# Kernel optimization log

Measured on AMD Instinct MI355X. Metric: run time of the kernel, lower is better.

## Reference

```python
import jax, jax.numpy as jnp
import numpy as np

EMB, HEADS, DEPTH, SEQ, BATCH = 256, 8, 4, 8192, 4
DH = EMB // HEADS  # 32
FF = 4 * EMB
EPS = 1e-5


def setup_inputs() -> dict:
    key = jax.random.key(0)
    ks = jax.random.split(key, 8)
    w = lambda k, shape: jax.random.normal(k, shape, dtype=jnp.float32) * 0.02
    D = DEPTH
    return {
        "x": jax.random.normal(ks[0], (BATCH, SEQ, EMB), dtype=jnp.float32),
        "Wq": w(ks[1], (D, EMB, EMB)),
        "Wk": w(ks[2], (D, EMB, EMB)),
        "Wv": w(ks[3], (D, EMB, EMB)),
        "Wo": w(ks[4], (D, EMB, EMB)),
        "bo": jnp.zeros((D, EMB), jnp.float32),
        "ln1_g": jnp.ones((D, EMB), jnp.float32),
        "ln1_b": jnp.zeros((D, EMB), jnp.float32),
        "W1": w(ks[5], (D, EMB, FF)),
        "b1": jnp.zeros((D, FF), jnp.float32),
        "W2": w(ks[6], (D, FF, EMB)),
        "b2": jnp.zeros((D, EMB), jnp.float32),
        "ln2_g": jnp.ones((D, EMB), jnp.float32),
        "ln2_b": jnp.zeros((D, EMB), jnp.float32),
    }


def _layernorm(x, g, b):
    mu = x.mean(-1, keepdims=True)
    var = ((x - mu) ** 2).mean(-1, keepdims=True)
    return (x - mu) * jax.lax.rsqrt(var + EPS) * g + b


def _linear_attn(x, Wq, Wk, Wv, Wo, bo):
    # lucidrains linear_attn: q,k scaled by d**-0.25; softmax q over feature dim,
    # k over sequence dim; context = k^T v (per head), out = q @ context.
    b, n, dm = x.shape
    split = lambda t: t.reshape(b, n, HEADS, DH).transpose(0, 2, 1, 3)  # -> bhnd
    scale = DH ** -0.25
    q = jax.nn.softmax(split(x @ Wq) * scale, axis=-1)   # over d
    k = jax.nn.softmax(split(x @ Wk) * scale, axis=-2)   # over n
    v = split(x @ Wv)
    context = jnp.einsum('bhnd,bhne->bhde', k, v)        # [b,h,d,d]
    out = jnp.einsum('bhnd,bhde->bhne', q, context)      # [b,h,n,d]
    out = out.transpose(0, 2, 1, 3).reshape(b, n, dm)
    return out @ Wo + bo


def _forward(x, Wq, Wk, Wv, Wo, bo, ln1_g, ln1_b, W1, b1, W2, b2, ln2_g, ln2_b):
    for i in range(DEPTH):
        h = _layernorm(x, ln1_g[i], ln1_b[i])
        x = x + _linear_attn(h, Wq[i], Wk[i], Wv[i], Wo[i], bo[i])
        h = _layernorm(x, ln2_g[i], ln2_b[i])
        x = x + (jax.nn.gelu(h @ W1[i] + b1[i], approximate=False) @ W2[i] + b2[i])
    return x


def reference(x, Wq, Wk, Wv, Wo, bo, ln1_g, ln1_b, W1, b1, W2, b2, ln2_g, ln2_b):
    return _forward(x, Wq, Wk, Wv, Wo, bo, ln1_g, ln1_b, W1, b1, W2, b2, ln2_g, ln2_b)
```

## Files before the change

kernel.cpp:

```cpp
#include <hip/hip_runtime.h>
#include <hip/hip_bf16.h>

typedef __attribute__((ext_vector_type(8))) short bf16x8;
typedef __attribute__((ext_vector_type(4))) float f32x4;

#define EMB 256
#define HEADS 8
#define DH 32
#define SEQ 8192
#define BATCH 4
#define NROWS (SEQ*BATCH)
#define FFD 1024
#define DEPTH 4
#define QKVN 768
#define SCALE 0.42044820762685725f
#define NCHUNK 128
#define ROWS_PER_CHUNK (SEQ/NCHUNK)

static __device__ __forceinline__ float bf2f(ushort u){
  union { unsigned int i; float f; } x; x.i = ((unsigned int)u) << 16; return x.f;
}
static __device__ __forceinline__ ushort f2bf(float f){
  union { __hip_bfloat16 h; ushort u; } cv;
  cv.h = __float2bfloat16(f);
  return cv.u;
}
static __device__ __forceinline__ float gelu_f(float v){
  float y = 0.7978845608028654f * (v + 0.044715f*v*v*v);
  float e = __expf(2.0f*y);
  return 0.5f*v*(1.0f + (1.0f - 2.0f/(e + 1.0f)));
}

static __device__ __forceinline__ void gload_lds16(const ushort* g, ushort* l){
  __builtin_amdgcn_global_load_lds(
      (const __attribute__((address_space(1))) unsigned int*)(uintptr_t)g,
      (__attribute__((address_space(3))) unsigned int*)(uintptr_t)l,
      16, 0, 0);
}

__global__ __launch_bounds__(256) void prep_weights(
    const float* __restrict__ Wq, const float* __restrict__ Wk,
    const float* __restrict__ Wv, const float* __restrict__ Wo,
    const float* __restrict__ W1, const float* __restrict__ W2,
    ushort* __restrict__ wqkv_t, ushort* __restrict__ wo_t,
    ushort* __restrict__ w1_t, ushort* __restrict__ w2_t)
{
  __shared__ float tile[32][33];
  int bid = blockIdx.x;
  int L = bid / 768, r = bid % 768;
  const float* src; ushort* dst; int K, N, tidx;
  if (r < 192){ int which = r >> 6; tidx = r & 63;
    src = (which==0?Wq:which==1?Wk:Wv) + (long)L*65536;
    dst = wqkv_t + (long)L*QKVN*EMB + which*EMB*EMB; K=256; N=256;
  } else if (r < 256){ tidx = r-192; src = Wo + (long)L*65536; dst = wo_t + (long)L*65536; K=256; N=256; }
  else if (r < 512){ tidx = r-256; src = W1 + (long)L*262144; dst = w1_t + (long)L*262144; K=256; N=1024; }
  else { tidx = r-512; src = W2 + (long)L*262144; dst = w2_t + (long)L*262144; K=1024; N=256; }
  int tn = N >> 5;
  int tk = tidx / tn, tj = tidx % tn;
  int k0 = tk*32, n0 = tj*32;
  int c = threadIdx.x & 31, r0 = threadIdx.x >> 5;
  #pragma unroll
  for (int i=0;i<4;i++){
    int rr = r0 + i*8;
    tile[rr][c] = src[(long)(k0+rr)*N + n0 + c];
  }
  __syncthreads();
  #pragma unroll
  for (int i=0;i<4;i++){
    int rr = r0 + i*8;
    dst[(long)(n0+rr)*K + k0 + c] = f2bf(tile[c][rr]);
  }
}

__global__ __launch_bounds__(256) void ln_kernel(const float* __restrict__ x,
    const float* __restrict__ g, const float* __restrict__ bb,
    ushort* __restrict__ h)
{
  int wid = threadIdx.x >> 6, lane = threadIdx.x & 63;
  long row = (long)blockIdx.x*4 + wid;
  const float4 xv = *(const float4*)(x + row*EMB + lane*4);
  float s = xv.x+xv.y+xv.z+xv.w;
  float s2 = xv.x*xv.x+xv.y*xv.y+xv.z*xv.z+xv.w*xv.w;
  #pragma unroll
  for (int m=1;m<64;m<<=1){ s += __shfl_xor(s,m,64); s2 += __shfl_xor(s2,m,64); }
  float mean = s * (1.0f/EMB);
  float inv = rsqrtf(s2*(1.0f/EMB) - mean*mean + 1e-5f);
  float4 gv = *(const float4*)(g + lane*4);
  float4 bv = *(const float4*)(bb + lane*4);
  ushort4 o;
  o.x = f2bf((xv.x-mean)*inv*gv.x + bv.x);
  o.y = f2bf((xv.y-mean)*inv*gv.y + bv.y);
  o.z = f2bf((xv.z-mean)*inv*gv.z + bv.z);
  o.w = f2bf((xv.w-mean)*inv*gv.w + bv.w);
  *(ushort4*)(h + row*EMB + lane*4) = o;
}

template<int MODE, int BM, int BN, int BK>
__global__ __launch_bounds__(512, 2) void gemm_bt(
    const ushort* __restrict__ A, const ushort* __restrict__ Bt,
    int M, int N, int K,
    const float* __restrict__ bias,
    const float* __restrict__ xin, float* __restrict__ xout,
    ushort* __restrict__ outb,
    const float* __restrict__ lng, const float* __restrict__ lnb)
{
  constexpr int NF = BN/64;
  constexpr int MR = BM/32;
  constexpr int MH = MR/4;
  constexpr int KK = BK/32;
  constexpr int CPR = BK/8;
  constexpr int AI = BM*BK/4096;
  constexpr int BI = BN*BK/4096;
  constexpr int TI = AI + BI;
  constexpr int NPH = KK*MH;
  __shared__ ushort LDSraw[2*BM*BK + 2*BN*BK];
  ushort* Abuf0 = LDSraw;
  ushort* Abuf1 = LDSraw + BM*BK;
  ushort* Bbuf0 = LDSraw + 2*BM*BK;
  ushort* Bbuf1 = LDSraw + 2*BM*BK + BN*BK;
  int t = threadIdx.x;
  int lane = t & 63, wid = t >> 6;
  int wr = wid >> 2, wc = wid & 3;
  int wrb = wr*(BM/2), wcb = wc*(BN/4);
  long rowA0 = (long)blockIdx.x * BM;
  long colB0 = (long)blockIdx.y * BN;
  const ushort* gA[AI]; int dA[AI];
  #pragma unroll
  for (int i=0;i<AI;i++){
    int l = i*512 + t;
    int row = l / CPR;
    int clog = (t % CPR) ^ (row & (CPR-1));
    gA[i] = A + (rowA0 + row)*(long)K + clog*8;
    dA[i] = l*8;
  }
  const ushort* gB[BI]; int dB[BI];
  #pragma unroll
  for (int i=0;i<BI;i++){
    int l = i*512 + t;
    int row = l / CPR;
    int clog = (t % CPR) ^ (row & (CPR-1));
    gB[i] = Bt + (colB0 + row)*(long)K + clog*8;
    dB[i] = l*8;
  }
  ushort* Ac = Abuf0; ushort* An = Abuf1;
  ushort* Bc = Bbuf0; ushort* Bn = Bbuf1;
  f32x4 acc[MR][NF] = {};
  int fr = lane & 15, cr4 = lane >> 4;
  int nsteps = K / BK;
  #pragma unroll
  for (int i=0;i<AI;i++) gload_lds16(gA[i], Ac + dA[i]);
  #pragma unroll
  for (int i=0;i<BI;i++) gload_lds16(gB[i], Bc + dB[i]);
  asm volatile("s_waitcnt vmcnt(0)" ::: "memory");
  __syncthreads();
  for (int s = 0; s < nsteps; ++s){
    bool pf = (s+1 < nsteps);
    long knext = (long)(s+1) * BK;
    #pragma unroll
    for (int kk=0; kk<KK; ++kk){
      int chunk = (((kk*4 + cr4)) ^ (fr & (CPR-1))) << 3;
      bf16x8 bv[NF];
      #pragma unroll
      for (int n=0;n<NF;n++)
        bv[n] = *(const bf16x8*)(Bc + (wcb + n*16 + fr)*BK + chunk);
      #pragma unroll
      for (int mh=0; mh<MH; ++mh){
        int sp = kk*MH + mh;
        bf16x8 av[4];
        #pragma unroll
        for (int m=0;m<4;m++)
          av[m] = *(const bf16x8*)(Ac + (wrb + (mh*4+m)*16 + fr)*BK + chunk);
        if (pf){
          #pragma unroll
          for (int j=0;j<TI;j++){
            if (j*NPH >= sp*TI && j*NPH < (sp+1)*TI){
              if (j < AI) gload_lds16(gA[j]+knext, An+dA[j]);
              else        gload_lds16(gB[j-AI]+knext, Bn+dB[j-AI]);
            }
          }
        }
        __builtin_amdgcn_s_setprio(1);
        #pragma unroll
        for (int m=0;m<4;m++){
          #pragma unroll
          for (int n=0;n<NF;n++)
            acc[mh*4+m][n] = __builtin_amdgcn_mfma_f32_16x16x32_bf16(av[m], bv[n], acc[mh*4+m][n], 0,0,0);
        }
        __builtin_amdgcn_s_setprio(0);
      }
    }
    asm volatile("s_waitcnt vmcnt(0)" ::: "memory");
    __syncthreads();
    ushort* tp;
    tp = Ac; Ac = An; An = tp;
    tp = Bc; Bc = Bn; Bn = tp;
  }
  constexpr int BNP = BN + 4;
  constexpr int ROUNDS = BM/32;
  constexpr int RPH = BM/64;
  float* bounce = (float*)LDSraw;
  int fq = lane >> 4;
  constexpr int TPR = BN/4;
  int rdrow = t / TPR;
  int rdcol = (t % TPR) * 4;
  constexpr int RPP = 512 / TPR;
  constexpr int PASSES = 32 / RPP;
  #pragma unroll
  for (int r = 0; r < ROUNDS; ++r){
    __syncthreads();
    if (wr == r / RPH){
      int mb = (r % RPH)*2;
      #pragma unroll
      for (int m4=0;m4<2;m4++){
        #pragma unroll
        for (int n=0;n<NF;n++){
          #pragma unroll
          for (int i=0;i<4;i++)
            bounce[(m4*16 + fq*4 + i)*BNP + wcb + n*16 + fr] = acc[mb+m4][n][i];
        }
      }
    }
    __syncthreads();
    long gr0 = rowA0 + r*32;
    #pragma unroll
    for (int p=0;p<PASSES;p++){
      int lr = p*RPP + rdrow;
      long gr = gr0 + lr;
      long gc = colB0 + rdcol;
      float4 v = *(float4*)&bounce[lr*BNP + rdcol];
      if (MODE==0){
        ushort4 o; o.x=f2bf(v.x); o.y=f2bf(v.y); o.z=f2bf(v.z); o.w=f2bf(v.w);
        *(ushort4*)&outb[gr*N + gc] = o;
      } else if (MODE==2){
        const float4 bv4 = *(const float4*)&bias[gc];
        ushort4 o;
        o.x = f2bf(gelu_f(v.x + bv4.x)); o.y = f2bf(gelu_f(v.y + bv4.y));
        o.z = f2bf(gelu_f(v.z + bv4.z)); o.w = f2bf(gelu_f(v.w + bv4.w));
        *(ushort4*)&outb[gr*N + gc] = o;
      } else {
        const float4 bv4 = *(const float4*)&bias[gc];
        const float4 xo  = *(const float4*)&xin[gr*N + gc];
        v.x += bv4.x + xo.x; v.y += bv4.y + xo.y;
        v.z += bv4.z + xo.z; v.w += bv4.w + xo.w;
        *(float4*)&xout[gr*N + gc] = v;
        float s1 = v.x+v.y+v.z+v.w;
        float s2 = v.x*v.x+v.y*v.y+v.z*v.z+v.w*v.w;
        #pragma unroll
        for (int mm=1;mm<64;mm<<=1){ s1 += __shfl_xor(s1,mm,64); s2 += __shfl_xor(s2,mm,64); }
        float mean = s1 * (1.0f/EMB);
        float inv = rsqrtf(s2*(1.0f/EMB) - mean*mean + 1e-5f);
        const float4 g4 = *(const float4*)&lng[gc];
        const float4 b4 = *(const float4*)&lnb[gc];
        ushort4 o;
        o.x = f2bf((v.x-mean)*inv*g4.x + b4.x);
        o.y = f2bf((v.y-mean)*inv*g4.y + b4.y);
        o.z = f2bf((v.z-mean)*inv*g4.z + b4.z);
        o.w = f2bf((v.w-mean)*inv*g4.w + b4.w);
        *(ushort4*)&outb[gr*EMB + gc] = o;
      }
    }
  }
}

__global__ __launch_bounds__(256) void colstats_partial(const ushort* __restrict__ qkv,
    float* __restrict__ pmax, float* __restrict__ psum)
{
  int ch = blockIdx.x, b = blockIdx.y;
  int t = threadIdx.x;
  const ushort* base = qkv + ((long)b*SEQ + (long)ch*ROWS_PER_CHUNK)*QKVN + EMB + t;
  float m[4] = {-1e30f,-1e30f,-1e30f,-1e30f};
  float s[4] = {0.f,0.f,0.f,0.f};
  #pragma unroll 2
  for (int n = 0; n < ROWS_PER_CHUNK; n += 4){
    #pragma unroll
    for (int j=0;j<4;j++){
      float v = bf2f(base[(long)(n+j)*QKVN]) * SCALE;
      float m2 = fmaxf(m[j], v);
      s[j] = s[j]*__expf(m[j]-m2) + __expf(v-m2);
      m[j] = m2;
    }
  }
  float M = fmaxf(fmaxf(m[0],m[1]), fmaxf(m[2],m[3]));
  float S = s[0]*__expf(m[0]-M) + s[1]*__expf(m[1]-M)
          + s[2]*__expf(m[2]-M) + s[3]*__expf(m[3]-M);
  long idx = ((long)b*NCHUNK + ch)*EMB + t;
  pmax[idx] = M; psum[idx] = S;
}

__global__ __launch_bounds__(256) void colstats_reduce(const float* __restrict__ pmax,
    const float* __restrict__ psum, float* __restrict__ kmax, float* __restrict__ ksum)
{
  int b = blockIdx.x, t = threadIdx.x;
  const float* pm = pmax + (long)b*NCHUNK*EMB + t;
  const float* ps = psum + (long)b*NCHUNK*EMB + t;
  float m = -1e30f, s = 0.f;
  for (int c = 0; c < NCHUNK; ++c){
    float cm = pm[(long)c*EMB], cs = ps[(long)c*EMB];
    float m2 = fmaxf(m, cm);
    s = s*__expf(m-m2) + cs*__expf(cm-m2);
    m = m2;
  }
  kmax[b*EMB + t] = m;
  ksum[b*EMB + t] = s;
}

__global__ __launch_bounds__(256) void ctx_partial(
    const ushort* __restrict__ qkv, const float* __restrict__ kmax,
    float* __restrict__ ctx_part)
{
  constexpr int LT = 72;
  __shared__ ushort ekT[32*LT];
  __shared__ ushort vvT[32*LT];
  int ch = blockIdx.x, h = blockIdx.y, b = blockIdx.z;
  int t = threadIdx.x, lane = t & 63, wid = t >> 6;
  long nbase = (long)b*SEQ + ch*512;
  int lrow = t >> 2, lseg = (t & 3) << 3;
  float km[8];
  #pragma unroll
  for (int j=0;j<8;j++) km[j] = kmax[b*256 + h*DH + lseg + j];
  int wstep = wid & 1, wdr = (wid >> 1) << 4;
  f32x4 acc0 = {}, acc1 = {};
  int frow = lane & 15, g8 = (lane >> 4) << 3;
  for (int st = 0; st < 8; ++st){
    long n0 = nbase + st*64;
    const ushort* gk = qkv + (n0 + lrow)*QKVN + EMB + h*DH + lseg;
    uint4 kv = *(const uint4*)gk;
    uint4 vv = *(const uint4*)(gk + EMB);
    __syncthreads();
    const ushort* kp = (const ushort*)&kv;
    const ushort* vp = (const ushort*)&vv;
    #pragma unroll
    for (int j=0;j<8;j++){
      float f = bf2f(kp[j])*SCALE;
      ekT[(lseg+j)*LT + lrow] = f2bf(__expf(f - km[j]));
      vvT[(lseg+j)*LT + lrow] = vp[j];
    }
    __syncthreads();
    bf16x8 afr = *(const bf16x8*)(ekT + (wdr + frow)*LT + wstep*32 + g8);
    bf16x8 bf0 = *(const bf16x8*)(vvT + frow*LT + wstep*32 + g8);
    bf16x8 bf1 = *(const bf16x8*)(vvT + (16 + frow)*LT + wstep*32 + g8);
    acc0 = __builtin_amdgcn_mfma_f32_16x16x32_bf16(afr, bf0, acc0, 0,0,0);
    acc1 = __builtin_amdgcn_mfma_f32_16x16x32_bf16(afr, bf1, acc1, 0,0,0);
  }
  int fq = lane >> 4;
  long pb = (((long)(b*HEADS+h))*32 + (ch*2+wstep))*1024;
  #pragma unroll
  for (int i=0;i<4;i++){
    ctx_part[pb + (wdr + fq*4 + i)*32 + frow] = acc0[i];
    ctx_part[pb + (wdr + fq*4 + i)*32 + 16 + frow] = acc1[i];
  }
}

__global__ __launch_bounds__(256) void ctx_reduce(const float* __restrict__ ctx_part,
    const float* __restrict__ ksum, ushort* __restrict__ ctxT)
{
  int bh = blockIdx.x; int b = bh >> 3, h = bh & 7;
  int t = threadIdx.x; int d = t >> 3, e4 = (t & 7) << 2;
  const float* p = ctx_part + (long)bh*32768 + d*32 + e4;
  float sx=0, sy=0, sz=0, sw=0;
  for (int c=0;c<32;c++){
    const float4 v = *(const float4*)(p + c*1024);
    sx+=v.x; sy+=v.y; sz+=v.z; sw+=v.w;
  }
  float inv = 1.0f / ksum[b*256 + h*DH + d];
  long base = (long)bh*1024;
  ctxT[base + (e4+0)*32 + d] = f2bf(sx*inv);
  ctxT[base + (e4+1)*32 + d] = f2bf(sy*inv);
  ctxT[base + (e4+2)*32 + d] = f2bf(sz*inv);
  ctxT[base + (e4+3)*32 + d] = f2bf(sw*inv);
}

__global__ __launch_bounds__(256) void attn_out(
    const ushort* __restrict__ qkv, const ushort* __restrict__ ctxT,
    ushort* __restrict__ ao)
{
  __shared__ ushort sq[4][16][264];
  int t = threadIdx.x, lane = t & 63, wid = t >> 6;
  long row0 = (long)blockIdx.x*64 + wid*16;
  int b = (int)(row0 / SEQ);
  int fr = lane & 15, g = lane >> 4;
  bf16x8 cf[8][2];
  #pragma unroll
  for (int h=0;h<8;h++){
    #pragma unroll
    for (int eh=0;eh<2;eh++)
      cf[h][eh] = *(const bf16x8*)(ctxT + ((long)(b*8+h)*32 + eh*16 + fr)*32 + g*8);
  }
  long gr = row0 + fr;
  #pragma unroll
  for (int hh=0;hh<2;hh++){
    int h = g*2 + hh;
    const ushort* qp = qkv + gr*QKVN + h*DH;
    union { uint4 v[4]; ushort u[32]; } qq;
    qq.v[0]=*(const uint4*)qp; qq.v[1]=*(const uint4*)(qp+8);
    qq.v[2]=*(const uint4*)(qp+16); qq.v[3]=*(const uint4*)(qp+24);
    float f[32]; float m = -1e30f;
    #pragma unroll
    for (int j=0;j<32;j++){ f[j] = bf2f(qq.u[j])*SCALE; m = fmaxf(m, f[j]); }
    float ssum = 0.f;
    #pragma unroll
    for (int j=0;j<32;j++){ f[j] = __expf(f[j]-m); ssum += f[j]; }
    float inv = 1.0f/ssum;
    union { uint4 v[4]; ushort u[32]; } oo;
    #pragma unroll
    for (int j=0;j<32;j++) oo.u[j] = f2bf(f[j]*inv);
    ushort* dst = &sq[wid][fr][h*DH];
    #pragma unroll
    for (int c2=0;c2<4;c2++) *(uint4*)(dst + c2*8) = oo.v[c2];
  }
  __syncthreads();
  #pragma unroll
  for (int h=0;h<8;h++){
    bf16x8 af = *(const bf16x8*)(&sq[wid][fr][h*DH + g*8]);
    f32x4 z = {};
    f32x4 o0 = __builtin_amdgcn_mfma_f32_16x16x32_bf16(af, cf[h][0], z, 0,0,0);
    f32x4 o1 = __builtin_amdgcn_mfma_f32_16x16x32_bf16(af, cf[h][1], z, 0,0,0);
    #pragma unroll
    for (int i=0;i<4;i++){
      long r = row0 + g*4 + i;
      ao[r*EMB + h*DH + fr]      = f2bf(o0[i]);
      ao[r*EMB + h*DH + 16 + fr] = f2bf(o1[i]);
    }
  }
}

extern "C" void kernel_launch(void* const* d_in, const int* in_sizes, int n_in,
                              void* d_out, int out_size, void* d_ws, size_t ws_size,
                              hipStream_t stream)
{
  const float* x_in = (const float*)d_in[0];
  const float* Wq  = (const float*)d_in[1];
  const float* Wk  = (const float*)d_in[2];
  const float* Wv  = (const float*)d_in[3];
  const float* Wo  = (const float*)d_in[4];
  const float* bo  = (const float*)d_in[5];
  const float* ln1g = (const float*)d_in[6];
  const float* ln1b = (const float*)d_in[7];
  const float* W1  = (const float*)d_in[8];
  const float* b1  = (const float*)d_in[9];
  const float* W2  = (const float*)d_in[10];
  const float* b2  = (const float*)d_in[11];
  const float* ln2g = (const float*)d_in[12];
  const float* ln2b = (const float*)d_in[13];
  float* x = (float*)d_out;

  char* ws = (char*)d_ws;
  ushort* h_buf  = (ushort*)ws;  ws += (long)NROWS*EMB*2;
  ushort* big    = (ushort*)ws;  ws += (long)NROWS*FFD*2;
  ushort* wqkv_t = (ushort*)ws;  ws += (long)DEPTH*QKVN*EMB*2;
  ushort* wo_t   = (ushort*)ws;  ws += (long)DEPTH*EMB*EMB*2;
  ushort* w1_t   = (ushort*)ws;  ws += (long)DEPTH*FFD*EMB*2;
  ushort* w2_t   = (ushort*)ws;  ws += (long)DEPTH*EMB*FFD*2;
  float*  kmax   = (float*)ws;   ws += (long)BATCH*EMB*4;
  float*  ksumv  = (float*)ws;   ws += (long)BATCH*EMB*4;
  float*  ctx_part = (float*)ws; ws += (long)BATCH*HEADS*32*1024*4;
  ushort* ctxT   = (ushort*)ws;  ws += (long)BATCH*HEADS*1024*2;
  float*  pmax   = (float*)ws;   ws += (long)BATCH*NCHUNK*EMB*4;
  float*  psum   = (float*)ws;   ws += (long)BATCH*NCHUNK*EMB*4;

  prep_weights<<<3072, 256, 0, stream>>>(Wq, Wk, Wv, Wo, W1, W2, wqkv_t, wo_t, w1_t, w2_t);
  ln_kernel<<<NROWS/4, 256, 0, stream>>>(x_in, ln1g, ln1b, h_buf);

  ushort* qkv = big;
  ushort* ffb = big;
  for (int L = 0; L < DEPTH; ++L){
    gemm_bt<0,128,128,64><<<dim3(NROWS/128, QKVN/128), 512, 0, stream>>>(
        h_buf, wqkv_t + (long)L*QKVN*EMB, NROWS, QKVN, EMB,
        nullptr, nullptr, nullptr, qkv, nullptr, nullptr);
    colstats_partial<<<dim3(NCHUNK, BATCH), 256, 0, stream>>>(qkv, pmax, psum);
    colstats_reduce<<<BATCH, 256, 0, stream>>>(pmax, psum, kmax, ksumv);
    ctx_partial<<<dim3(16, HEADS, BATCH), 256, 0, stream>>>(qkv, kmax, ctx_part);
    ctx_reduce<<<32, 256, 0, stream>>>(ctx_part, ksumv, ctxT);
    attn_out<<<NROWS/64, 256, 0, stream>>>(qkv, ctxT, h_buf);
    gemm_bt<3,128,256,64><<<dim3(NROWS/128, 1), 512, 0, stream>>>(
        h_buf, wo_t + (long)L*EMB*EMB, NROWS, EMB, EMB,
        bo + L*EMB, (L==0 ? x_in : x), x, h_buf,
        ln2g + L*EMB, ln2b + L*EMB);
    gemm_bt<2,128,128,64><<<dim3(NROWS/128, FFD/128), 512, 0, stream>>>(
        h_buf, w1_t + (long)L*FFD*EMB, NROWS, FFD, EMB,
        b1 + L*FFD, nullptr, nullptr, ffb, nullptr, nullptr);
    int Ln = (L+1 < DEPTH) ? (L+1) : 0;
    gemm_bt<3,128,256,64><<<dim3(NROWS/128, 1), 512, 0, stream>>>(
        ffb, w2_t + (long)L*EMB*FFD, NROWS, EMB, FFD,
        b2 + L*EMB, x, x, h_buf,
        ln1g + Ln*EMB, ln1b + Ln*EMB);
  }
}
```

Before: 659.9 us.

## Add row-resident GEMM keeping full-K A tile in LDS for QKV and FF1

Adds a GEMM kernel where each block loads its 128-row A tile with the full K=256 into LDS once, then sweeps every output column chunk, double-buffering 128x128 B tiles. The QKV and W1 projections now use it with 256 blocks instead of a 2D grid. The aim is to stop the A panel being reloaded from global memory once per column tile. The cost is a large LDS footprint (about 64KB A, 64KB B and a 17KB bounce buffer), fewer and longer blocks, and serialized epilogue syncs that may limit occupancy.

New measurement: 669.2 us. Within noise of the previous version (+1.4%).

```diff
diff --git a/kernel.cpp b/kernel.cpp
--- a/kernel.cpp
+++ b/kernel.cpp
@@ -93,6 +93,131 @@
   o.z = f2bf((xv.z-mean)*inv*gv.z + bv.z);
   o.w = f2bf((xv.w-mean)*inv*gv.w + bv.w);
   *(ushort4*)(h + row*EMB + lane*4) = o;
+}
+
+template<int MODE, int NCH>
+__global__ __launch_bounds__(512, 2) void gemm_arow(
+    const ushort* __restrict__ A, const ushort* __restrict__ Bt,
+    int N, const float* __restrict__ bias, ushort* __restrict__ outb)
+{
+  constexpr int K = 256;
+  constexpr int NS = 2*NCH;
+  __shared__ ushort As[128*256];
+  __shared__ ushort Bs0[128*128];
+  __shared__ ushort Bs1[128*128];
+  __shared__ float bounce[32*132];
+  int t = threadIdx.x;
+  int lane = t & 63, wid = t >> 6;
+  int wr = wid >> 2, wc = wid & 3;
+  int wrb = wr*64, wcb = wc*32;
+  long rowA0 = (long)blockIdx.x * 128;
+  int fr = lane & 15, cr4 = lane >> 4, fq = lane >> 4;
+  const ushort* gA[8]; int dA[8];
+  #pragma unroll
+  for (int i=0;i<8;i++){
+    int l = i*512 + t;
+    int row = l >> 5;
+    int clog = (l & 31) ^ (row & 31);
+    gA[i] = A + (rowA0 + row)*(long)K + clog*8;
+    dA[i] = l*8;
+  }
+  long boff[4]; int dB[4];
+  #pragma unroll
+  for (int i=0;i<4;i++){
+    int l = i*512 + t;
+    int rc = l >> 4;
+    int clog = (l & 15) ^ (rc & 15);
+    boff[i] = (long)rc*K + clog*8;
+    dB[i] = l*8;
+  }
+  #pragma unroll
+  for (int i=0;i<8;i++) gload_lds16(gA[i], As + dA[i]);
+  #pragma unroll
+  for (int i=0;i<4;i++) gload_lds16(Bt + boff[i], Bs0 + dB[i]);
+  asm volatile("s_waitcnt vmcnt(0)" ::: "memory");
+  __syncthreads();
+  f32x4 acc[4][2] = {};
+  for (int s = 0; s < NS; ++s){
+    int kh = s & 1, j = s >> 1;
+    ushort* Bc = (s & 1) ? Bs1 : Bs0;
+    ushort* Bn = (s & 1) ? Bs0 : Bs1;
+    #pragma unroll
+    for (int kk=0; kk<4; ++kk){
+      if (kk==0 && s+1 < NS){
+        long nbase = (long)((s+1)>>1)*128*K + ((s+1)&1)*128;
+        #pragma unroll
+        for (int i=0;i<4;i++) gload_lds16(Bt + nbase + boff[i], Bn + dB[i]);
+      }
+      bf16x8 bv[2];
+      #pragma unroll
+      for (int n=0;n<2;n++){
+        int rc2 = wcb + n*16 + fr;
+        bv[n] = *(const bf16x8*)(Bc + rc2*128 + (((kk*4+cr4) ^ (rc2 & 15)) << 3));
+      }
+      bf16x8 av[4];
+      #pragma unroll
+      for (int m=0;m<4;m++){
+        int rr = wrb + m*16 + fr;
+        av[m] = *(const bf16x8*)(As + rr*256 + (((kh*16+kk*4+cr4) ^ (rr & 31)) << 3));
+      }
+      __builtin_amdgcn_s_setprio(1);
+      #pragma unroll
+      for (int m=0;m<4;m++){
+        #pragma unroll
+        for (int n=0;n<2;n++)
+          acc[m][n] = __builtin_amdgcn_mfma_f32_16x16x32_bf16(av[m], bv[n], acc[m][n], 0,0,0);
+      }
+      __builtin_amdgcn_s_setprio(0);
+    }
+    if (kh == 1){
+      int rdrow = t >> 5;
+      int rdcol = (t & 31) * 4;
+      long gc = (long)j*128 + rdcol;
+      #pragma unroll
+      for (int r = 0; r < 4; ++r){
+        __syncthreads();
+        if (wr == (r>>1)){
+          int mb = (r&1)*2;
+          #pragma unroll
+          for (int m4=0;m4<2;m4++){
+            #pragma unroll
+            for (int n=0;n<2;n++){
+              #pragma unroll
+              for (int i=0;i<4;i++)
+                bounce[(m4*16 + fq*4 + i)*132 + wcb + n*16 + fr] = acc[mb+m4][n][i];
+            }
+          }
+        }
+        __syncthreads();
+        #pragma unroll
+        for (int p=0;p<2;p++){
+          int lr = p*16 + rdrow;
+          long gr = rowA0 + r*32 + lr;
+          float4 v = *(float4*)&bounce[lr*132 + rdcol];
+          if (MODE==0){
+            ushort4 o; o.x=f2bf(v.x); o.y=f2bf(v.y); o.z=f2bf(v.z); o.w=f2bf(v.w);
+            *(ushort4*)&outb[gr*N + gc] = o;
+          } else {
+            const float4 bv4 = *(const float4*)&bias[gc];
+            ushort4 o;
+            o.x = f2bf(gelu_f(v.x + bv4.x)); o.y = f2bf(gelu_f(v.y + bv4.y));
+            o.z = f2bf(gelu_f(v.z + bv4.z)); o.w = f2bf(gelu_f(v.w + bv4.w));
+            *(ushort4*)&outb[gr*N + gc] = o;
+          }
+        }
+      }
+      #pragma unroll
+      for (int m=0;m<4;m++){
+        #pragma unroll
+        for (int n=0;n<2;n++)
+          acc[m][n] = (f32x4){0.f,0.f,0.f,0.f};
+      }
+    }
+    if (s+1 < NS){
+      asm volatile("s_waitcnt vmcnt(0)" ::: "memory");
+      __syncthreads();
+    }
+  }
 }
 
 template<int MODE, int BM, int BN, int BK>
@@ -464,9 +589,8 @@
   ushort* qkv = big;
   ushort* ffb = big;
   for (int L = 0; L < DEPTH; ++L){
-    gemm_bt<0,128,128,64><<<dim3(NROWS/128, QKVN/128), 512, 0, stream>>>(
-        h_buf, wqkv_t + (long)L*QKVN*EMB, NROWS, QKVN, EMB,
-        nullptr, nullptr, nullptr, qkv, nullptr, nullptr);
+    gemm_arow<0,6><<<256, 512, 0, stream>>>(
+        h_buf, wqkv_t + (long)L*QKVN*EMB, QKVN, nullptr, qkv);
     colstats_partial<<<dim3(NCHUNK, BATCH), 256, 0, stream>>>(qkv, pmax, psum);
     colstats_reduce<<<BATCH, 256, 0, stream>>>(pmax, psum, kmax, ksumv);
     ctx_partial<<<dim3(16, HEADS, BATCH), 256, 0, stream>>>(qkv, kmax, ctx_part);
@@ -476,9 +600,8 @@
         h_buf, wo_t + (long)L*EMB*EMB, NROWS, EMB, EMB,
         bo + L*EMB, (L==0 ? x_in : x), x, h_buf,
         ln2g + L*EMB, ln2b + L*EMB);
-    gemm_bt<2,128,128,64><<<dim3(NROWS/128, FFD/128), 512, 0, stream>>>(
-        h_buf, w1_t + (long)L*FFD*EMB, NROWS, FFD, EMB,
-        b1 + L*FFD, nullptr, nullptr, ffb, nullptr, nullptr);
+    gemm_arow<2,8><<<256, 512, 0, stream>>>(
+        h_buf, w1_t + (long)L*FFD*EMB, FFD, b1 + L*FFD, ffb);
     int Ln = (L+1 < DEPTH) ? (L+1) : 0;
     gemm_bt<3,128,256,64><<<dim3(NROWS/128, 1), 512, 0, stream>>>(
         ffb, w2_t + (long)L*EMB*FFD, NROWS, EMB, FFD,
```

## Add register-direct MFMA GEMM without LDS staging for QKV and FF1 projections

Applied to the files above, without the earlier changes.

Adds a gemm_direct kernel that loads A and B fragments straight from global memory into registers, with one-step prefetch, and runs 16x16x32 bf16 MFMAs without staging operands in shared memory. LDS is used only to transpose the output for coalesced stores, with the GELU bias epilogue fused in. It replaces the LDS-tiled gemm_bt for the K=256 QKV and W1 GEMMs to cut LDS traffic and barriers. In exchange, each wave reads its operands directly from global memory, so it depends on L2 reuse and loses the shared-tile reuse between waves.

New measurement: 877.9 us. 33.0% more time.

```diff
diff --git a/kernel.cpp b/kernel.cpp
--- a/kernel.cpp
+++ b/kernel.cpp
@@ -93,6 +93,90 @@
   o.z = f2bf((xv.z-mean)*inv*gv.z + bv.z);
   o.w = f2bf((xv.w-mean)*inv*gv.w + bv.w);
   *(ushort4*)(h + row*EMB + lane*4) = o;
+}
+
+template<int MODE, int K>
+__global__ __launch_bounds__(256) void gemm_direct(
+    const ushort* __restrict__ A, const ushort* __restrict__ Bt,
+    int N, const float* __restrict__ bias, ushort* __restrict__ outb)
+{
+  __shared__ float wb[4][16*68];
+  int t = threadIdx.x, lane = t & 63, wid = t >> 6;
+  int wr = wid >> 1, wc = wid & 1;
+  long rowA0 = (long)blockIdx.x*128 + wr*64;
+  long colB0 = (long)blockIdx.y*128 + wc*64;
+  int fr = lane & 15, cr4 = lane >> 4;
+  const ushort* ap[4]; const ushort* bp[4];
+  #pragma unroll
+  for (int m=0;m<4;m++) ap[m] = A + (rowA0 + m*16 + fr)*(long)K + cr4*8;
+  #pragma unroll
+  for (int n=0;n<4;n++) bp[n] = Bt + (colB0 + n*16 + fr)*(long)K + cr4*8;
+  f32x4 acc[4][4] = {};
+  constexpr int NKS = K/32;
+  bf16x8 a0[4], b0[4];
+  #pragma unroll
+  for (int m=0;m<4;m++) a0[m] = *(const bf16x8*)(ap[m]);
+  #pragma unroll
+  for (int n=0;n<4;n++) b0[n] = *(const bf16x8*)(bp[n]);
+  #pragma unroll
+  for (int ks=0; ks<NKS; ++ks){
+    bf16x8 a1[4], b1[4];
+    if (ks+1 < NKS){
+      int off = (ks+1)*32;
+      #pragma unroll
+      for (int m=0;m<4;m++) a1[m] = *(const bf16x8*)(ap[m] + off);
+      #pragma unroll
+      for (int n=0;n<4;n++) b1[n] = *(const bf16x8*)(bp[n] + off);
+    }
+    __builtin_amdgcn_s_setprio(1);
+    #pragma unroll
+    for (int m=0;m<4;m++){
+      #pragma unroll
+      for (int n=0;n<4;n++)
+        acc[m][n] = __builtin_amdgcn_mfma_f32_16x16x32_bf16(a0[m], b0[n], acc[m][n], 0,0,0);
+    }
+    __builtin_amdgcn_s_setprio(0);
+    #pragma unroll
+    for (int m=0;m<4;m++) a0[m] = a1[m];
+    #pragma unroll
+    for (int n=0;n<4;n++) b0[n] = b1[n];
+  }
+  int rr = lane >> 2, c0 = (lane & 3) * 16;
+  #pragma unroll
+  for (int m=0;m<4;m++){
+    #pragma unroll
+    for (int n=0;n<4;n++){
+      #pragma unroll
+      for (int i=0;i<4;i++)
+        wb[wid][(cr4*4 + i)*68 + n*16 + fr] = acc[m][n][i];
+    }
+    asm volatile("s_waitcnt lgkmcnt(0)" ::: "memory");
+    float4 v0 = *(float4*)&wb[wid][rr*68 + c0];
+    float4 v1 = *(float4*)&wb[wid][rr*68 + c0 + 4];
+    float4 v2 = *(float4*)&wb[wid][rr*68 + c0 + 8];
+    float4 v3 = *(float4*)&wb[wid][rr*68 + c0 + 12];
+    asm volatile("s_waitcnt lgkmcnt(0)" ::: "memory");
+    long gr = rowA0 + m*16 + rr;
+    long gc = colB0 + c0;
+    ushort o[16];
+    float vv[16] = {v0.x,v0.y,v0.z,v0.w, v1.x,v1.y,v1.z,v1.w,
+                    v2.x,v2.y,v2.z,v2.w, v3.x,v3.y,v3.z,v3.w};
+    if (MODE==0){
+      #pragma unroll
+      for (int j=0;j<16;j++) o[j] = f2bf(vv[j]);
+    } else {
+      const float4 bb0 = *(const float4*)&bias[gc];
+      const float4 bb1 = *(const float4*)&bias[gc+4];
+      const float4 bb2 = *(const float4*)&bias[gc+8];
+      const float4 bb3 = *(const float4*)&bias[gc+12];
+      float bvv[16] = {bb0.x,bb0.y,bb0.z,bb0.w, bb1.x,bb1.y,bb1.z,bb1.w,
+                       bb2.x,bb2.y,bb2.z,bb2.w, bb3.x,bb3.y,bb3.z,bb3.w};
+      #pragma unroll
+      for (int j=0;j<16;j++) o[j] = f2bf(gelu_f(vv[j] + bvv[j]));
+    }
+    *(uint4*)&outb[gr*N + gc]     = *(uint4*)&o[0];
+    *(uint4*)&outb[gr*N + gc + 8] = *(uint4*)&o[8];
+  }
 }
 
 template<int MODE, int BM, int BN, int BK>
@@ -464,9 +548,8 @@
   ushort* qkv = big;
   ushort* ffb = big;
   for (int L = 0; L < DEPTH; ++L){
-    gemm_bt<0,128,128,64><<<dim3(NROWS/128, QKVN/128), 512, 0, stream>>>(
-        h_buf, wqkv_t + (long)L*QKVN*EMB, NROWS, QKVN, EMB,
-        nullptr, nullptr, nullptr, qkv, nullptr, nullptr);
+    gemm_direct<0,256><<<dim3(NROWS/128, QKVN/128), 256, 0, stream>>>(
+        h_buf, wqkv_t + (long)L*QKVN*EMB, QKVN, nullptr, qkv);
     colstats_partial<<<dim3(NCHUNK, BATCH), 256, 0, stream>>>(qkv, pmax, psum);
     colstats_reduce<<<BATCH, 256, 0, stream>>>(pmax, psum, kmax, ksumv);
     ctx_partial<<<dim3(16, HEADS, BATCH), 256, 0, stream>>>(qkv, kmax, ctx_part);
@@ -476,9 +559,8 @@
         h_buf, wo_t + (long)L*EMB*EMB, NROWS, EMB, EMB,
         bo + L*EMB, (L==0 ? x_in : x), x, h_buf,
         ln2g + L*EMB, ln2b + L*EMB);
-    gemm_bt<2,128,128,64><<<dim3(NROWS/128, FFD/128), 512, 0, stream>>>(
-        h_buf, w1_t + (long)L*FFD*EMB, NROWS, FFD, EMB,
-        b1 + L*FFD, nullptr, nullptr, ffb, nullptr, nullptr);
+    gemm_direct<2,256><<<dim3(NROWS/128, FFD/128), 256, 0, stream>>>(
+        h_buf, w1_t + (long)L*FFD*EMB, FFD, b1 + L*FFD, ffb);
     int Ln = (L+1 < DEPTH) ? (L+1) : 0;
     gemm_bt<3,128,256,64><<<dim3(NROWS/128, 1), 512, 0, stream>>>(
         ffb, w2_t + (long)L*EMB*FFD, NROWS, EMB, FFD,
```
